# Kernel tuning notes

Measured on AMD Instinct MI355X. Metric: run time of the kernel, lower is better.

Reference implementation:

```python
import jax, jax.numpy as jnp
import numpy as np

B, S, D = 2, 2048, 1024
H = 16
HD = D // H  # 64


def setup_inputs() -> dict:
    key = jax.random.key(0)
    ks = jax.random.split(key, 7)
    return {
        "query": jax.random.normal(ks[0], (B, S, D), dtype=jnp.float32),
        "sin_q": jax.random.uniform(ks[1], (1, 1, S, HD), dtype=jnp.float32),
        "cos_q": jax.random.uniform(ks[2], (1, 1, S, HD), dtype=jnp.float32),
        "sin_k": jax.random.uniform(ks[3], (1, 1, S, HD), dtype=jnp.float32),
        "cos_k": jax.random.uniform(ks[4], (1, 1, S, HD), dtype=jnp.float32),
        # params: fused QKV proj [D, 3D] (x @ w_in) and output proj [D, D]
        "w_in": jax.random.normal(ks[5], (D, 3 * D), dtype=jnp.float32) / np.sqrt(D),
        "w_out": jax.random.normal(ks[6], (D, D), dtype=jnp.float32) / np.sqrt(D),
    }


def _rotate_half(x):
    x1, x2 = jnp.split(x, 2, axis=-1)
    return jnp.concatenate([-x2, x1], axis=-1)


def _rope(x, sin, cos):
    # prefix = N - sin_len == 0 here, so plain RoPE over the full sequence
    return x * cos + _rotate_half(x) * sin


def reference(query, sin_q, cos_q, sin_k, cos_k, w_in, w_out):
    b, s, d = query.shape
    scale = 1.0 / np.sqrt(HD)
    # fused QKV projection
    qkv = query @ w_in  # [B,S,3D]
    q, k, v = jnp.split(qkv, 3, axis=-1)

    def to_heads(x):
        return x.reshape(b, s, H, HD).transpose(0, 2, 1, 3)  # [B,H,S,HD]

    q, k, v = to_heads(q), to_heads(k), to_heads(v)
    q = _rope(q, sin_q, cos_q)
    k = _rope(k, sin_k, cos_k)
    # causal SDPA
    scores = jnp.einsum("bhqd,bhkd->bhqk", q, k) * scale  # [B,H,S,S]
    causal = jnp.tril(jnp.ones((s, s), dtype=bool))
    scores = jnp.where(causal, scores, jnp.finfo(scores.dtype).min)
    attn = jax.nn.softmax(scores, axis=-1)
    out = jnp.einsum("bhqk,bhkd->bhqd", attn, v)  # [B,H,S,HD]
    out = out.transpose(0, 2, 1, 3).reshape(b, s, d)
    return out @ w_out
```

## Files before the change

### kernel.cpp

```cpp
#include <hip/hip_runtime.h>
#include <hip/hip_bf16.h>
#include <math.h>

#define BB 2
#define SS 2048
#define DD 1024
#define HH 16
#define HDD 64

typedef float f32x4 __attribute__((ext_vector_type(4)));
typedef short s16x8 __attribute__((ext_vector_type(8)));
typedef unsigned short u16x8 __attribute__((ext_vector_type(8)));

__device__ inline unsigned short f2bf(float x) {
  unsigned u = __float_as_uint(x);
  unsigned r = u + 0x7fff + ((u >> 16) & 1);
  return (unsigned short)(r >> 16);
}
__device__ inline float bf2f(unsigned short h) {
  return __uint_as_float(((unsigned)h) << 16);
}

__global__ __launch_bounds__(256) void cast_bf16_kernel(const float* __restrict__ X,
                                                        unsigned short* __restrict__ Xb,
                                                        int n4) {
  int i = blockIdx.x * 256 + threadIdx.x;
  if (i >= n4) return;
  float4 v = ((const float4*)X)[i];
  ushort4 h;
  h.x = f2bf(v.x); h.y = f2bf(v.y); h.z = f2bf(v.z); h.w = f2bf(v.w);
  ((ushort4*)Xb)[i] = h;
}

__global__ __launch_bounds__(256) void split_transpose_kernel(
    const float* __restrict__ W, unsigned short* __restrict__ WTh,
    unsigned short* __restrict__ WTl, int K, int N) {
  __shared__ float tile[64][65];
  const int k0 = blockIdx.y * 64, n0 = blockIdx.x * 64;
  const int t = threadIdx.x;
  const int c = t & 63, rq = t >> 6;
#pragma unroll
  for (int u = 0; u < 16; ++u) {
    int r = u * 4 + rq;
    tile[r][c] = W[(size_t)(k0 + r) * N + n0 + c];
  }
  __syncthreads();
#pragma unroll
  for (int u = 0; u < 16; ++u) {
    int nl = u * 4 + rq;
    float v = tile[c][nl];
    unsigned short h = f2bf(v);
    unsigned short l = f2bf(v - bf2f(h));
    size_t o = (size_t)(n0 + nl) * K + k0 + c;
    WTh[o] = h;
    WTl[o] = l;
  }
}

#define GLDS16(g, l)                                                        \
  __builtin_amdgcn_global_load_lds(                                         \
      (const __attribute__((address_space(1))) unsigned int*)(const void*)(g), \
      (__attribute__((address_space(3))) unsigned int*)(l), 16, 0, 0)

#define GEMM2T_PRE(Ab, BTh, BTl, Kdim)                                      \
  const int t = threadIdx.x;                                                \
  const int bm = blockIdx.y * 128;                                          \
  const int bn = blockIdx.x * 128;                                          \
  const int w = t >> 6, lane = t & 63;                                      \
  const int wrow = (w >> 1) * 64, wcol = (w & 1) * 64;                      \
  const int l15 = lane & 15, l4 = lane >> 4, l7 = lane & 7;                 \
  int ldsoff[4];                                                            \
  const unsigned short* pA[4];                                              \
  const unsigned short* pBh[4];                                             \
  const unsigned short* pBl[4];                                             \
  _Pragma("unroll")                                                         \
  for (int cc = 0; cc < 4; ++cc) {                                          \
    int tp = t + cc * 256;                                                  \
    int srow = tp >> 3;                                                     \
    int gq = (tp & 7) ^ (srow & 7);                                         \
    ldsoff[cc] = tp * 8;                                                    \
    pA[cc]  = (Ab)  + (size_t)(bm + srow) * (Kdim) + gq * 8;                \
    pBh[cc] = (BTh) + (size_t)(bn + srow) * (Kdim) + gq * 8;                \
    pBl[cc] = (BTl) + (size_t)(bn + srow) * (Kdim) + gq * 8;                \
  }                                                                         \
  f32x4 acc[4][4];                                                          \
  const f32x4 z = {0.f, 0.f, 0.f, 0.f};                                     \
  _Pragma("unroll")                                                         \
  for (int m = 0; m < 4; ++m)                                               \
    _Pragma("unroll")                                                       \
    for (int n = 0; n < 4; ++n) acc[m][n] = z;                              \
  for (int k0 = 0; k0 < (Kdim); k0 += 64) {                                 \
    __syncthreads();                                                        \
    _Pragma("unroll")                                                       \
    for (int cc = 0; cc < 4; ++cc) {                                        \
      GLDS16(pA[cc] + k0, &As_b[ldsoff[cc]]);                               \
      GLDS16(pBh[cc] + k0, &Bs_h[ldsoff[cc]]);                              \
      GLDS16(pBl[cc] + k0, &Bs_l[ldsoff[cc]]);                              \
    }                                                                       \
    __syncthreads();                                                        \
    _Pragma("unroll")                                                       \
    for (int ks = 0; ks < 2; ++ks) {                                        \
      const int sw = ((ks * 4 + l4) ^ l7) * 8;                              \
      s16x8 a[4], bh[4], bl[4];                                             \
      _Pragma("unroll")                                                     \
      for (int m = 0; m < 4; ++m)                                           \
        a[m] = *(const s16x8*)&As_b[(wrow + m * 16 + l15) * 64 + sw];       \
      _Pragma("unroll")                                                     \
      for (int n = 0; n < 4; ++n) {                                         \
        int idx = (wcol + n * 16 + l15) * 64 + sw;                          \
        bh[n] = *(const s16x8*)&Bs_h[idx];                                  \
        bl[n] = *(const s16x8*)&Bs_l[idx];                                  \
      }                                                                     \
      _Pragma("unroll")                                                     \
      for (int m = 0; m < 4; ++m)                                           \
        _Pragma("unroll")                                                   \
        for (int n = 0; n < 4; ++n) {                                       \
          acc[m][n] = __builtin_amdgcn_mfma_f32_16x16x32_bf16(a[m], bh[n], acc[m][n], 0, 0, 0); \
          acc[m][n] = __builtin_amdgcn_mfma_f32_16x16x32_bf16(a[m], bl[n], acc[m][n], 0, 0, 0); \
        }                                                                   \
    }                                                                       \
  }

__global__ __launch_bounds__(256) void gemm_qkv_rope_kernel(
    const unsigned short* __restrict__ Ab,
    const unsigned short* __restrict__ BTh, const unsigned short* __restrict__ BTl,
    const float* __restrict__ sin_q, const float* __restrict__ cos_q,
    const float* __restrict__ sin_k, const float* __restrict__ cos_k,
    unsigned short* __restrict__ Qhi, unsigned short* __restrict__ Qlo,
    unsigned short* __restrict__ Khi, unsigned short* __restrict__ Vt) {
  __shared__ __align__(16) unsigned short As_b[128 * 64];
  __shared__ __align__(16) unsigned short Bs_h[128 * 64];
  __shared__ __align__(16) unsigned short Bs_l[128 * 64];
  GEMM2T_PRE(Ab, BTh, BTl, DD)

  const int region = bn >> 10;
  const int hloc = ((bn & 1023) + wcol) >> 6;
  const float QSC = 0.125f * 1.44269504088896340736f;

  if (region == 0) {
#pragma unroll
    for (int m = 0; m < 4; ++m) {
      const int row0 = bm + wrow + m * 16 + l4 * 4;
#pragma unroll
      for (int r = 0; r < 4; ++r) {
        const int row = row0 + r, b = row >> 11, s = row & 2047;
        const size_t ob = ((size_t)(b * HH + hloc) * SS + s) * HDD;
        const float* cq = cos_q + s * HDD;
        const float* sq = sin_q + s * HDD;
#pragma unroll
        for (int np = 0; np < 2; ++np) {
          const int d1 = np * 16 + l15;
          float x1 = acc[m][np][r], x2 = acc[m][np + 2][r];
          float q1 = (x1 * cq[d1] - x2 * sq[d1]) * QSC;
          float q2 = (x2 * cq[d1 + 32] + x1 * sq[d1 + 32]) * QSC;
          unsigned short h1 = f2bf(q1), h2 = f2bf(q2);
          Qhi[ob + d1] = h1;      Qlo[ob + d1] = f2bf(q1 - bf2f(h1));
          Qhi[ob + d1 + 32] = h2; Qlo[ob + d1 + 32] = f2bf(q2 - bf2f(h2));
        }
      }
    }
  } else if (region == 1) {
#pragma unroll
    for (int m = 0; m < 4; ++m) {
      const int row0 = bm + wrow + m * 16 + l4 * 4;
#pragma unroll
      for (int r = 0; r < 4; ++r) {
        const int row = row0 + r, b = row >> 11, s = row & 2047;
        const size_t ob = ((size_t)(b * HH + hloc) * SS + s) * HDD;
        const float* ck = cos_k + s * HDD;
        const float* sk = sin_k + s * HDD;
#pragma unroll
        for (int np = 0; np < 2; ++np) {
          const int d1 = np * 16 + l15;
          float x1 = acc[m][np][r], x2 = acc[m][np + 2][r];
          Khi[ob + d1]      = f2bf(x1 * ck[d1] - x2 * sk[d1]);
          Khi[ob + d1 + 32] = f2bf(x2 * ck[d1 + 32] + x1 * sk[d1 + 32]);
        }
      }
    }
  } else {
#pragma unroll
    for (int m = 0; m < 4; ++m) {
      const int row0 = bm + wrow + m * 16 + l4 * 4;
      const int b = row0 >> 11, s0 = row0 & 2047;
#pragma unroll
      for (int n = 0; n < 4; ++n) {
        const int d = n * 16 + l15;
        ushort4 v4;
        v4.x = f2bf(acc[m][n][0]);
        v4.y = f2bf(acc[m][n][1]);
        v4.z = f2bf(acc[m][n][2]);
        v4.w = f2bf(acc[m][n][3]);
        *(ushort4*)&Vt[((size_t)(b * HH + hloc) * HDD + d) * SS + s0] = v4;
      }
    }
  }
}

__global__ __launch_bounds__(256) void gemm_out_kernel(
    const unsigned short* __restrict__ Ab,
    const unsigned short* __restrict__ BTh, const unsigned short* __restrict__ BTl,
    float* __restrict__ C) {
  __shared__ __align__(16) unsigned short As_b[128 * 64];
  __shared__ __align__(16) unsigned short Bs_h[128 * 64];
  __shared__ __align__(16) unsigned short Bs_l[128 * 64];
  GEMM2T_PRE(Ab, BTh, BTl, DD)

#pragma unroll
  for (int m = 0; m < 4; ++m)
#pragma unroll
    for (int n = 0; n < 4; ++n) {
      f32x4 v = acc[m][n];
      int col = bn + wcol + n * 16 + l15;
      int row0 = bm + wrow + m * 16 + l4 * 4;
#pragma unroll
      for (int r = 0; r < 4; ++r) C[(size_t)(row0 + r) * DD + col] = v[r];
    }
}


#define ATTN_TILE(QH, QL, OO, LS, MM, MASKED, CUR)                               \
  do {                                                                           \
    f32x4 sc[4];                                                                 \
    sc[0] = z; sc[1] = z; sc[2] = z; sc[3] = z;                                  \
    __builtin_amdgcn_s_setprio(1);                                               \
    _Pragma("unroll")                                                            \
    for (int kc = 0; kc < 2; ++kc) {                                             \
      const int swz = ((kc * 4 + l4) ^ l7) * 8;                                  \
      _Pragma("unroll")                                                          \
      for (int n = 0; n < 4; ++n) {                                              \
        const int idx = (n * 16 + l15) * 64 + swz;                               \
        s16x8 kh = *(const s16x8*)&Ks[CUR][idx];                                 \
        sc[n] = __builtin_amdgcn_mfma_f32_16x16x32_bf16(QH[kc], kh, sc[n], 0, 0, 0); \
        sc[n] = __builtin_amdgcn_mfma_f32_16x16x32_bf16(QL[kc], kh, sc[n], 0, 0, 0); \
      }                                                                          \
    }                                                                            \
    __builtin_amdgcn_s_setprio(0);                                               \
    if (MASKED) {                                                                \
      _Pragma("unroll")                                                          \
      for (int n = 0; n < 4; ++n)                                                \
        _Pragma("unroll")                                                        \
        for (int r = 0; r < 4; ++r)                                              \
          if (n * 16 + l15 > w * 16 + l4 * 4 + r) sc[n][r] = -INFINITY;          \
    }                                                                            \
    float pm[4];                                                                 \
    _Pragma("unroll")                                                            \
    for (int r = 0; r < 4; ++r) {                                                \
      float tm = fmaxf(fmaxf(sc[0][r], sc[1][r]), fmaxf(sc[2][r], sc[3][r]));    \
      tm = fmaxf(tm, __shfl_xor(tm, 1));                                         \
      tm = fmaxf(tm, __shfl_xor(tm, 2));                                         \
      tm = fmaxf(tm, __shfl_xor(tm, 4));                                         \
      tm = fmaxf(tm, __shfl_xor(tm, 8));                                         \
      pm[r] = tm;                                                                 \
    }                                                                            \
    float growth = fmaxf(fmaxf(pm[0] - MM[0], pm[1] - MM[1]),                    \
                         fmaxf(pm[2] - MM[2], pm[3] - MM[3]));                   \
    if (!__all(growth <= 8.f)) {                                                 \
      _Pragma("unroll")                                                          \
      for (int r = 0; r < 4; ++r) {                                              \
        float mn = fmaxf(MM[r], pm[r]);                                          \
        float corr = __builtin_amdgcn_exp2f(MM[r] - mn);                         \
        MM[r] = mn;                                                              \
        OO[0][r] *= corr; OO[1][r] *= corr; OO[2][r] *= corr; OO[3][r] *= corr;  \
        LS[r] *= corr;                                                           \
      }                                                                          \
    }                                                                            \
    _Pragma("unroll")                                                            \
    for (int r = 0; r < 4; ++r) {                                                \
      const int pr = (w * 16 + l4 * 4 + r) * 72;                                 \
      _Pragma("unroll")                                                          \
      for (int n = 0; n < 4; ++n)                                                \
        Ps[pr + n * 16 + l15] = f2bf(__builtin_amdgcn_exp2f(sc[n][r] - MM[r]));  \
    }                                                                            \
    const int prow = (w * 16 + l15) * 72;                                        \
    __builtin_amdgcn_s_setprio(1);                                               \
    _Pragma("unroll")                                                            \
    for (int c = 0; c < 2; ++c) {                                                \
      s16x8 pa = *(const s16x8*)&Ps[prow + c * 32 + 8 * l4];                     \
      const int swz = ((c * 4 + l4) ^ l7) * 8;                                   \
      _Pragma("unroll")                                                          \
      for (int n = 0; n < 4; ++n) {                                              \
        s16x8 vb = *(const s16x8*)&Vs[CUR][(n * 16 + l15) * 64 + swz];           \
        OO[n] = __builtin_amdgcn_mfma_f32_16x16x32_bf16(pa, vb, OO[n], 0, 0, 0); \
      }                                                                          \
      LS = __builtin_amdgcn_mfma_f32_16x16x32_bf16(pa, ones, LS, 0, 0, 0);       \
    }                                                                            \
    __builtin_amdgcn_s_setprio(0);                                               \
  } while (0)

#define ATTN_EPI(OO, LS, QI)                                                     \
  do {                                                                           \
    _Pragma("unroll")                                                            \
    for (int r = 0; r < 4; ++r) {                                                \
      const float inv = 1.f / LS[r];                                             \
      const int orow = (QI) * 64 + w * 16 + l4 * 4 + r;                          \
      const size_t ob = ((size_t)b * SS + orow) * DD + h * HDD + l15;            \
      _Pragma("unroll")                                                          \
      for (int n = 0; n < 4; ++n)                                                \
        Ohi[ob + n * 16] = f2bf(OO[n][r] * inv);                                 \
    }                                                                            \
  } while (0)

__global__ __launch_bounds__(256) void attn_mfma_kernel(
    const unsigned short* __restrict__ Qhi, const unsigned short* __restrict__ Qlo,
    const unsigned short* __restrict__ Khi_g, const unsigned short* __restrict__ Vt_g,
    unsigned short* __restrict__ Ohi) {
  __shared__ __align__(16) unsigned short Ks[2][64 * 64];
  __shared__ __align__(16) unsigned short Vs[2][64 * 64];
  __shared__ __align__(16) unsigned short Ps[64 * 72];

  const int t = threadIdx.x;
  const int lane = t & 63;
  const int w = t >> 6;
  const int p = blockIdx.x;
  const int qiA = 31 - p, qiB = p;
  const int bh = blockIdx.y;
  const int b = bh >> 4, h = bh & 15;
  const int l15 = lane & 15, l4 = lane >> 4, l7 = lane & 7;

  s16x8 qhA[2], qlA[2], qhB[2], qlB[2];
  {
    const int rowA = qiA * 64 + w * 16 + l15;
    const unsigned short* qb = Qhi + ((size_t)bh * SS + rowA) * HDD + 8 * l4;
    const unsigned short* qc = Qlo + ((size_t)bh * SS + rowA) * HDD + 8 * l4;
    qhA[0] = *(const s16x8*)(qb);
    qhA[1] = *(const s16x8*)(qb + 32);
    qlA[0] = *(const s16x8*)(qc);
    qlA[1] = *(const s16x8*)(qc + 32);
    const int rowB = qiB * 64 + w * 16 + l15;
    const unsigned short* qd = Qhi + ((size_t)bh * SS + rowB) * HDD + 8 * l4;
    const unsigned short* qe = Qlo + ((size_t)bh * SS + rowB) * HDD + 8 * l4;
    qhB[0] = *(const s16x8*)(qd);
    qhB[1] = *(const s16x8*)(qd + 32);
    qlB[0] = *(const s16x8*)(qe);
    qlB[1] = *(const s16x8*)(qe + 32);
  }

  int lds[2];
  size_t koff[2], voff[2];
#pragma unroll
  for (int c = 0; c < 2; ++c) {
    int G = t + c * 256;
    int row = G >> 3, g = G & 7;
    int gs = g ^ (row & 7);
    lds[c] = G * 8;
    koff[c] = ((size_t)bh * SS + row) * HDD + gs * 8;
    voff[c] = ((size_t)bh * HDD + row) * SS + gs * 8;
  }

  const f32x4 z = {0.f, 0.f, 0.f, 0.f};
  f32x4 oA[4], oB[4], lsA = z, lsB = z;
#pragma unroll
  for (int n = 0; n < 4; ++n) { oA[n] = z; oB[n] = z; }
  float mA[4], mB[4];
#pragma unroll
  for (int r = 0; r < 4; ++r) { mA[r] = -INFINITY; mB[r] = -INFINITY; }

  const short one_bf = (short)0x3F80;
  const s16x8 ones = {one_bf, one_bf, one_bf, one_bf, one_bf, one_bf, one_bf, one_bf};

#pragma unroll
  for (int c = 0; c < 2; ++c) {
    GLDS16(Khi_g + koff[c], &Ks[0][lds[c]]);
    GLDS16(Vt_g + voff[c], &Vs[0][lds[c]]);
  }
  __syncthreads();

  int cur = 0;
  for (int kt = 0; kt <= qiA; ++kt) {
    if (kt < qiA) {
      const size_t ka = (size_t)(kt + 1) * 64 * HDD;
      const size_t va = (size_t)(kt + 1) * 64;
      const int nxt = cur ^ 1;
#pragma unroll
      for (int c = 0; c < 2; ++c) {
        GLDS16(Khi_g + ka + koff[c], &Ks[nxt][lds[c]]);
        GLDS16(Vt_g + va + voff[c], &Vs[nxt][lds[c]]);
      }
    }
    ATTN_TILE(qhA, qlA, oA, lsA, mA, kt == qiA, cur);
    if (kt <= qiB) ATTN_TILE(qhB, qlB, oB, lsB, mB, kt == qiB, cur);
    __syncthreads();
    cur ^= 1;
  }

  ATTN_EPI(oA, lsA, qiA);
  ATTN_EPI(oB, lsB, qiB);
}

extern "C" void kernel_launch(void* const* d_in, const int* in_sizes, int n_in,
                              void* d_out, int out_size, void* d_ws, size_t ws_size,
                              hipStream_t stream) {
  const float* query = (const float*)d_in[0];
  const float* sin_q = (const float*)d_in[1];
  const float* cos_q = (const float*)d_in[2];
  const float* sin_k = (const float*)d_in[3];
  const float* cos_k = (const float*)d_in[4];
  const float* w_in  = (const float*)d_in[5];
  const float* w_out = (const float*)d_in[6];
  float* out = (float*)d_out;

  const int M = BB * SS;
  const size_t MD = (size_t)M * DD;

  unsigned char* ws = (unsigned char*)d_ws;
  size_t off = 0;
  unsigned short* Qb  = (unsigned short*)(ws + off); off += MD * 2;
  unsigned short* B1h = (unsigned short*)(ws + off); off += (size_t)DD * 3 * DD * 2;
  unsigned short* B1l = (unsigned short*)(ws + off); off += (size_t)DD * 3 * DD * 2;
  unsigned short* B2h = (unsigned short*)(ws + off); off += (size_t)DD * DD * 2;
  unsigned short* B2l = (unsigned short*)(ws + off); off += (size_t)DD * DD * 2;
  unsigned short* Qhi = (unsigned short*)(ws + off); off += MD * 2;
  unsigned short* Qlo = (unsigned short*)(ws + off); off += MD * 2;
  unsigned short* Khi = (unsigned short*)(ws + off); off += MD * 2;
  unsigned short* Vt  = (unsigned short*)(ws + off); off += MD * 2;
  unsigned short* Ohi = (unsigned short*)(ws + off); off += MD * 2;

  {
    int n4 = (int)(MD / 4);
    cast_bf16_kernel<<<(n4 + 255) / 256, 256, 0, stream>>>(query, Qb, n4);
    split_transpose_kernel<<<dim3(3 * DD / 64, DD / 64), 256, 0, stream>>>(w_in, B1h, B1l, DD, 3 * DD);
    split_transpose_kernel<<<dim3(DD / 64, DD / 64), 256, 0, stream>>>(w_out, B2h, B2l, DD, DD);
  }
  {
    dim3 grid((3 * DD) / 128, M / 128);
    gemm_qkv_rope_kernel<<<grid, 256, 0, stream>>>(
        Qb, B1h, B1l, sin_q, cos_q, sin_k, cos_k, Qhi, Qlo, Khi, Vt);
  }
  {
    dim3 grid(SS / 128, BB * HH);
    attn_mfma_kernel<<<grid, 256, 0, stream>>>(Qhi, Qlo, Khi, Vt, Ohi);
  }
  {
    dim3 grid(DD / 128, M / 128);
    gemm_out_kernel<<<grid, 256, 0, stream>>>(Ohi, B2h, B2l, out);
  }
}
```

Measured before the change: 248.3 us.

## Widen attention KV tiles to 128 keys with register-staged prefetch

The attention kernel now processes 128 keys per iteration instead of 64, halving loop trips and block barriers. The double-buffered direct global-to-LDS loads are replaced by a single LDS buffer, with the next tile prefetched into registers and written to LDS between two barriers. The V layout and swizzle are adapted to 128-wide rows. The trade-off is higher register pressure (8 score fragments plus staged K and V) and extra masked work on diagonal tiles, since 64-row query tiles are now paired with 128-key tiles.

```diff
diff --git a/kernel.cpp b/kernel.cpp
--- a/kernel.cpp
+++ b/kernel.cpp
@@ -219,18 +219,18 @@
 }
 
 
-#define ATTN_TILE(QH, QL, OO, LS, MM, MASKED, CUR)                               \
+#define ATTN_TILE128(QH, QL, OO, LS, MM, MASKED, QI)                             \
   do {                                                                           \
-    f32x4 sc[4];                                                                 \
-    sc[0] = z; sc[1] = z; sc[2] = z; sc[3] = z;                                  \
+    f32x4 sc[8];                                                                 \
+    _Pragma("unroll")                                                            \
+    for (int n = 0; n < 8; ++n) sc[n] = z;                                       \
     __builtin_amdgcn_s_setprio(1);                                               \
     _Pragma("unroll")                                                            \
     for (int kc = 0; kc < 2; ++kc) {                                             \
       const int swz = ((kc * 4 + l4) ^ l7) * 8;                                  \
       _Pragma("unroll")                                                          \
-      for (int n = 0; n < 4; ++n) {                                              \
-        const int idx = (n * 16 + l15) * 64 + swz;                               \
-        s16x8 kh = *(const s16x8*)&Ks[CUR][idx];                                 \
+      for (int n = 0; n < 8; ++n) {                                              \
+        s16x8 kh = *(const s16x8*)&Ks[(n * 16 + l15) * 64 + swz];                \
         sc[n] = __builtin_amdgcn_mfma_f32_16x16x32_bf16(QH[kc], kh, sc[n], 0, 0, 0); \
         sc[n] = __builtin_amdgcn_mfma_f32_16x16x32_bf16(QL[kc], kh, sc[n], 0, 0, 0); \
       }                                                                          \
@@ -238,15 +238,18 @@
     __builtin_amdgcn_s_setprio(0);                                               \
     if (MASKED) {                                                                \
       _Pragma("unroll")                                                          \
-      for (int n = 0; n < 4; ++n)                                                \
+      for (int n = 0; n < 8; ++n) {                                              \
+        const int colg = ktb + n * 16 + l15;                                     \
         _Pragma("unroll")                                                        \
         for (int r = 0; r < 4; ++r)                                              \
-          if (n * 16 + l15 > w * 16 + l4 * 4 + r) sc[n][r] = -INFINITY;          \
+          if (colg > (QI) * 64 + rowl + r) sc[n][r] = -INFINITY;                 \
+      }                                                                          \
     }                                                                            \
     float pm[4];                                                                 \
     _Pragma("unroll")                                                            \
     for (int r = 0; r < 4; ++r) {                                                \
-      float tm = fmaxf(fmaxf(sc[0][r], sc[1][r]), fmaxf(sc[2][r], sc[3][r]));    \
+      float tm = fmaxf(fmaxf(fmaxf(sc[0][r], sc[1][r]), fmaxf(sc[2][r], sc[3][r])), \
+                       fmaxf(fmaxf(sc[4][r], sc[5][r]), fmaxf(sc[6][r], sc[7][r]))); \
       tm = fmaxf(tm, __shfl_xor(tm, 1));                                         \
       tm = fmaxf(tm, __shfl_xor(tm, 2));                                         \
       tm = fmaxf(tm, __shfl_xor(tm, 4));                                         \
@@ -267,20 +270,21 @@
     }                                                                            \
     _Pragma("unroll")                                                            \
     for (int r = 0; r < 4; ++r) {                                                \
-      const int pr = (w * 16 + l4 * 4 + r) * 72;                                 \
-      _Pragma("unroll")                                                          \
-      for (int n = 0; n < 4; ++n)                                                \
+      const int pr = (rowl + r) * 136;                                           \
+      _Pragma("unroll")                                                          \
+      for (int n = 0; n < 8; ++n)                                                \
         Ps[pr + n * 16 + l15] = f2bf(__builtin_amdgcn_exp2f(sc[n][r] - MM[r]));  \
     }                                                                            \
-    const int prow = (w * 16 + l15) * 72;                                        \
+    const int prow = (w * 16 + l15) * 136;                                       \
     __builtin_amdgcn_s_setprio(1);                                               \
     _Pragma("unroll")                                                            \
-    for (int c = 0; c < 2; ++c) {                                                \
+    for (int c = 0; c < 4; ++c) {                                                \
       s16x8 pa = *(const s16x8*)&Ps[prow + c * 32 + 8 * l4];                     \
-      const int swz = ((c * 4 + l4) ^ l7) * 8;                                   \
+      const int q = c * 4 + l4;                                                  \
+      const int rq = (q & 8) | ((q ^ l7) & 7);                                   \
       _Pragma("unroll")                                                          \
       for (int n = 0; n < 4; ++n) {                                              \
-        s16x8 vb = *(const s16x8*)&Vs[CUR][(n * 16 + l15) * 64 + swz];           \
+        s16x8 vb = *(const s16x8*)&Vs[(n * 16 + l15) * 128 + rq * 8];            \
         OO[n] = __builtin_amdgcn_mfma_f32_16x16x32_bf16(pa, vb, OO[n], 0, 0, 0); \
       }                                                                          \
       LS = __builtin_amdgcn_mfma_f32_16x16x32_bf16(pa, ones, LS, 0, 0, 0);       \
@@ -293,7 +297,7 @@
     _Pragma("unroll")                                                            \
     for (int r = 0; r < 4; ++r) {                                                \
       const float inv = 1.f / LS[r];                                             \
-      const int orow = (QI) * 64 + w * 16 + l4 * 4 + r;                          \
+      const int orow = (QI) * 64 + rowl + r;                                     \
       const size_t ob = ((size_t)b * SS + orow) * DD + h * HDD + l15;            \
       _Pragma("unroll")                                                          \
       for (int n = 0; n < 4; ++n)                                                \
@@ -305,9 +309,9 @@
     const unsigned short* __restrict__ Qhi, const unsigned short* __restrict__ Qlo,
     const unsigned short* __restrict__ Khi_g, const unsigned short* __restrict__ Vt_g,
     unsigned short* __restrict__ Ohi) {
-  __shared__ __align__(16) unsigned short Ks[2][64 * 64];
-  __shared__ __align__(16) unsigned short Vs[2][64 * 64];
-  __shared__ __align__(16) unsigned short Ps[64 * 72];
+  __shared__ __align__(16) unsigned short Ks[128 * 64];
+  __shared__ __align__(16) unsigned short Vs[64 * 128];
+  __shared__ __align__(16) unsigned short Ps[64 * 136];
 
   const int t = threadIdx.x;
   const int lane = t & 63;
@@ -317,6 +321,7 @@
   const int bh = blockIdx.y;
   const int b = bh >> 4, h = bh & 15;
   const int l15 = lane & 15, l4 = lane >> 4, l7 = lane & 7;
+  const int rowl = w * 16 + l4 * 4;
 
   s16x8 qhA[2], qlA[2], qhB[2], qlB[2];
   {
@@ -336,16 +341,19 @@
     qlB[1] = *(const s16x8*)(qe + 32);
   }
 
-  int lds[2];
-  size_t koff[2], voff[2];
-#pragma unroll
-  for (int c = 0; c < 2; ++c) {
-    int G = t + c * 256;
-    int row = G >> 3, g = G & 7;
-    int gs = g ^ (row & 7);
-    lds[c] = G * 8;
-    koff[c] = ((size_t)bh * SS + row) * HDD + gs * 8;
-    voff[c] = ((size_t)bh * HDD + row) * SS + gs * 8;
+  int ldsk[4], ldsv[4];
+  size_t koff[4], voff[4];
+#pragma unroll
+  for (int cc = 0; cc < 4; ++cc) {
+    const int G = t + cc * 256;
+    const int krow = G >> 3, kg = G & 7;
+    const int kgs = kg ^ (krow & 7);
+    ldsk[cc] = G * 8;
+    koff[cc] = ((size_t)bh * SS + krow) * HDD + kgs * 8;
+    const int vrow = G >> 4, vg = G & 15;
+    const int vgs = (vg & 8) | ((vg ^ vrow) & 7);
+    ldsv[cc] = G * 8;
+    voff[cc] = ((size_t)bh * HDD + vrow) * SS + vgs * 8;
   }
 
   const f32x4 z = {0.f, 0.f, 0.f, 0.f};
@@ -359,29 +367,45 @@
   const short one_bf = (short)0x3F80;
   const s16x8 ones = {one_bf, one_bf, one_bf, one_bf, one_bf, one_bf, one_bf, one_bf};
 
-#pragma unroll
-  for (int c = 0; c < 2; ++c) {
-    GLDS16(Khi_g + koff[c], &Ks[0][lds[c]]);
-    GLDS16(Vt_g + voff[c], &Vs[0][lds[c]]);
+  const int ktA_max = qiA >> 1;
+  const int ktB_max = qiB >> 1;
+
+  u16x8 kreg[4], vreg[4];
+#pragma unroll
+  for (int cc = 0; cc < 4; ++cc) {
+    kreg[cc] = *(const u16x8*)(Khi_g + koff[cc]);
+    vreg[cc] = *(const u16x8*)(Vt_g + voff[cc]);
+  }
+#pragma unroll
+  for (int cc = 0; cc < 4; ++cc) {
+    *(u16x8*)&Ks[ldsk[cc]] = kreg[cc];
+    *(u16x8*)&Vs[ldsv[cc]] = vreg[cc];
   }
   __syncthreads();
 
-  int cur = 0;
-  for (int kt = 0; kt <= qiA; ++kt) {
-    if (kt < qiA) {
-      const size_t ka = (size_t)(kt + 1) * 64 * HDD;
-      const size_t va = (size_t)(kt + 1) * 64;
-      const int nxt = cur ^ 1;
-#pragma unroll
-      for (int c = 0; c < 2; ++c) {
-        GLDS16(Khi_g + ka + koff[c], &Ks[nxt][lds[c]]);
-        GLDS16(Vt_g + va + voff[c], &Vs[nxt][lds[c]]);
+  for (int kt = 0; kt <= ktA_max; ++kt) {
+    const int ktb = kt << 7;
+    const bool pf = kt < ktA_max;
+    if (pf) {
+      const size_t ka = (size_t)(kt + 1) * 128 * HDD;
+      const size_t va = (size_t)(kt + 1) * 128;
+#pragma unroll
+      for (int cc = 0; cc < 4; ++cc) {
+        kreg[cc] = *(const u16x8*)(Khi_g + ka + koff[cc]);
+        vreg[cc] = *(const u16x8*)(Vt_g + va + voff[cc]);
       }
     }
-    ATTN_TILE(qhA, qlA, oA, lsA, mA, kt == qiA, cur);
-    if (kt <= qiB) ATTN_TILE(qhB, qlB, oB, lsB, mB, kt == qiB, cur);
-    __syncthreads();
-    cur ^= 1;
+    ATTN_TILE128(qhA, qlA, oA, lsA, mA, kt == ktA_max, qiA);
+    if (kt <= ktB_max) ATTN_TILE128(qhB, qlB, oB, lsB, mB, kt == ktB_max, qiB);
+    if (pf) {
+      __syncthreads();
+#pragma unroll
+      for (int cc = 0; cc < 4; ++cc) {
+        *(u16x8*)&Ks[ldsk[cc]] = kreg[cc];
+        *(u16x8*)&Vs[ldsv[cc]] = vreg[cc];
+      }
+      __syncthreads();
+    }
   }
 
   ATTN_EPI(oA, lsA, qiA);
```

New measurement: 266.9 us. 1.07x slower.

## Interleave the two query tiles' MFMAs so they share K/V fragment loads

Applied to the files above, without the earlier changes.

Restructures the attention inner loop so the QK^T and PV MFMAs for both query tiles (A and B) run in one pass. Each K and V fragment read from LDS now feeds both tiles, and the softmax for each tile writes to its own P buffer. The block index is also remapped so batch-head pairs are spread differently across workgroups, which may change L2 locality. In exchange the kernel needs more registers and a second P buffer in LDS, and the divergent doB checks sit inside the unrolled loops, which could lower occupancy.

```diff
diff --git a/kernel.cpp b/kernel.cpp
--- a/kernel.cpp
+++ b/kernel.cpp
@@ -219,34 +219,12 @@
 }
 
 
-#define ATTN_TILE(QH, QL, OO, LS, MM, MASKED, CUR)                               \
+#define ATTN_SM(SC, OO, LS, MM, PS)                                              \
   do {                                                                           \
-    f32x4 sc[4];                                                                 \
-    sc[0] = z; sc[1] = z; sc[2] = z; sc[3] = z;                                  \
-    __builtin_amdgcn_s_setprio(1);                                               \
-    _Pragma("unroll")                                                            \
-    for (int kc = 0; kc < 2; ++kc) {                                             \
-      const int swz = ((kc * 4 + l4) ^ l7) * 8;                                  \
-      _Pragma("unroll")                                                          \
-      for (int n = 0; n < 4; ++n) {                                              \
-        const int idx = (n * 16 + l15) * 64 + swz;                               \
-        s16x8 kh = *(const s16x8*)&Ks[CUR][idx];                                 \
-        sc[n] = __builtin_amdgcn_mfma_f32_16x16x32_bf16(QH[kc], kh, sc[n], 0, 0, 0); \
-        sc[n] = __builtin_amdgcn_mfma_f32_16x16x32_bf16(QL[kc], kh, sc[n], 0, 0, 0); \
-      }                                                                          \
-    }                                                                            \
-    __builtin_amdgcn_s_setprio(0);                                               \
-    if (MASKED) {                                                                \
-      _Pragma("unroll")                                                          \
-      for (int n = 0; n < 4; ++n)                                                \
-        _Pragma("unroll")                                                        \
-        for (int r = 0; r < 4; ++r)                                              \
-          if (n * 16 + l15 > w * 16 + l4 * 4 + r) sc[n][r] = -INFINITY;          \
-    }                                                                            \
     float pm[4];                                                                 \
     _Pragma("unroll")                                                            \
     for (int r = 0; r < 4; ++r) {                                                \
-      float tm = fmaxf(fmaxf(sc[0][r], sc[1][r]), fmaxf(sc[2][r], sc[3][r]));    \
+      float tm = fmaxf(fmaxf(SC[0][r], SC[1][r]), fmaxf(SC[2][r], SC[3][r]));    \
       tm = fmaxf(tm, __shfl_xor(tm, 1));                                         \
       tm = fmaxf(tm, __shfl_xor(tm, 2));                                         \
       tm = fmaxf(tm, __shfl_xor(tm, 4));                                         \
@@ -270,22 +248,8 @@
       const int pr = (w * 16 + l4 * 4 + r) * 72;                                 \
       _Pragma("unroll")                                                          \
       for (int n = 0; n < 4; ++n)                                                \
-        Ps[pr + n * 16 + l15] = f2bf(__builtin_amdgcn_exp2f(sc[n][r] - MM[r]));  \
+        PS[pr + n * 16 + l15] = f2bf(__builtin_amdgcn_exp2f(SC[n][r] - MM[r]));  \
     }                                                                            \
-    const int prow = (w * 16 + l15) * 72;                                        \
-    __builtin_amdgcn_s_setprio(1);                                               \
-    _Pragma("unroll")                                                            \
-    for (int c = 0; c < 2; ++c) {                                                \
-      s16x8 pa = *(const s16x8*)&Ps[prow + c * 32 + 8 * l4];                     \
-      const int swz = ((c * 4 + l4) ^ l7) * 8;                                   \
-      _Pragma("unroll")                                                          \
-      for (int n = 0; n < 4; ++n) {                                              \
-        s16x8 vb = *(const s16x8*)&Vs[CUR][(n * 16 + l15) * 64 + swz];           \
-        OO[n] = __builtin_amdgcn_mfma_f32_16x16x32_bf16(pa, vb, OO[n], 0, 0, 0); \
-      }                                                                          \
-      LS = __builtin_amdgcn_mfma_f32_16x16x32_bf16(pa, ones, LS, 0, 0, 0);       \
-    }                                                                            \
-    __builtin_amdgcn_s_setprio(0);                                               \
   } while (0)
 
 #define ATTN_EPI(OO, LS, QI)                                                     \
@@ -307,14 +271,16 @@
     unsigned short* __restrict__ Ohi) {
   __shared__ __align__(16) unsigned short Ks[2][64 * 64];
   __shared__ __align__(16) unsigned short Vs[2][64 * 64];
-  __shared__ __align__(16) unsigned short Ps[64 * 72];
+  __shared__ __align__(16) unsigned short PsA[64 * 72];
+  __shared__ __align__(16) unsigned short PsB[64 * 72];
 
   const int t = threadIdx.x;
   const int lane = t & 63;
   const int w = t >> 6;
-  const int p = blockIdx.x;
+  const int flat = (int)blockIdx.y * 16 + (int)blockIdx.x;
+  const int p = flat >> 5;
+  const int bh = ((flat & 7) << 2) | ((flat >> 3) & 3);
   const int qiA = 31 - p, qiB = p;
-  const int bh = blockIdx.y;
   const int b = bh >> 4, h = bh & 15;
   const int l15 = lane & 15, l4 = lane >> 4, l7 = lane & 7;
 
@@ -368,6 +334,7 @@
 
   int cur = 0;
   for (int kt = 0; kt <= qiA; ++kt) {
+    const bool doB = kt <= qiB;
     if (kt < qiA) {
       const size_t ka = (size_t)(kt + 1) * 64 * HDD;
       const size_t va = (size_t)(kt + 1) * 64;
@@ -378,8 +345,68 @@
         GLDS16(Vt_g + va + voff[c], &Vs[nxt][lds[c]]);
       }
     }
-    ATTN_TILE(qhA, qlA, oA, lsA, mA, kt == qiA, cur);
-    if (kt <= qiB) ATTN_TILE(qhB, qlB, oB, lsB, mB, kt == qiB, cur);
+
+    f32x4 scA[4], scB[4];
+#pragma unroll
+    for (int n = 0; n < 4; ++n) { scA[n] = z; scB[n] = z; }
+    __builtin_amdgcn_s_setprio(1);
+#pragma unroll
+    for (int kc = 0; kc < 2; ++kc) {
+      const int swz = ((kc * 4 + l4) ^ l7) * 8;
+#pragma unroll
+      for (int n = 0; n < 4; ++n) {
+        const s16x8 kh = *(const s16x8*)&Ks[cur][(n * 16 + l15) * 64 + swz];
+        scA[n] = __builtin_amdgcn_mfma_f32_16x16x32_bf16(qhA[kc], kh, scA[n], 0, 0, 0);
+        scA[n] = __builtin_amdgcn_mfma_f32_16x16x32_bf16(qlA[kc], kh, scA[n], 0, 0, 0);
+        if (doB) {
+          scB[n] = __builtin_amdgcn_mfma_f32_16x16x32_bf16(qhB[kc], kh, scB[n], 0, 0, 0);
+          scB[n] = __builtin_amdgcn_mfma_f32_16x16x32_bf16(qlB[kc], kh, scB[n], 0, 0, 0);
+        }
+      }
+    }
+    __builtin_amdgcn_s_setprio(0);
+
+    if (kt == qiA) {
+#pragma unroll
+      for (int n = 0; n < 4; ++n)
+#pragma unroll
+        for (int r = 0; r < 4; ++r)
+          if (n * 16 + l15 > w * 16 + l4 * 4 + r) scA[n][r] = -INFINITY;
+    }
+    if (kt == qiB) {
+#pragma unroll
+      for (int n = 0; n < 4; ++n)
+#pragma unroll
+        for (int r = 0; r < 4; ++r)
+          if (n * 16 + l15 > w * 16 + l4 * 4 + r) scB[n][r] = -INFINITY;
+    }
+
+    ATTN_SM(scA, oA, lsA, mA, PsA);
+    if (doB) ATTN_SM(scB, oB, lsB, mB, PsB);
+
+    const int prow = (w * 16 + l15) * 72;
+    __builtin_amdgcn_s_setprio(1);
+#pragma unroll
+    for (int c = 0; c < 2; ++c) {
+      const s16x8 paA = *(const s16x8*)&PsA[prow + c * 32 + 8 * l4];
+      const int swz = ((c * 4 + l4) ^ l7) * 8;
+#pragma unroll
+      for (int n = 0; n < 4; ++n) {
+        const s16x8 vb = *(const s16x8*)&Vs[cur][(n * 16 + l15) * 64 + swz];
+        oA[n] = __builtin_amdgcn_mfma_f32_16x16x32_bf16(paA, vb, oA[n], 0, 0, 0);
+        if (doB) {
+          const s16x8 paB = *(const s16x8*)&PsB[prow + c * 32 + 8 * l4];
+          oB[n] = __builtin_amdgcn_mfma_f32_16x16x32_bf16(paB, vb, oB[n], 0, 0, 0);
+        }
+      }
+      lsA = __builtin_amdgcn_mfma_f32_16x16x32_bf16(paA, ones, lsA, 0, 0, 0);
+      if (doB) {
+        const s16x8 paB = *(const s16x8*)&PsB[prow + c * 32 + 8 * l4];
+        lsB = __builtin_amdgcn_mfma_f32_16x16x32_bf16(paB, ones, lsB, 0, 0, 0);
+      }
+    }
+    __builtin_amdgcn_s_setprio(0);
+
     __syncthreads();
     cur ^= 1;
   }
```

Measured after the change: 258.8 us. +4.2%, slower.
